# Performance work log

Measured on AMD Instinct MI355X. Metric: run time of the kernel, lower is better.

The kernel has to match this reference:

```python
import jax, jax.numpy as jnp
import numpy as np

N = 100000      # entity nodes
E = 1000000     # edges per relation
D_IN = 256
HID = 128
EPS = 1e-16     # PyG softmax denominator eps
NEG_SLOPE = 0.2 # GATConv default leaky_relu slope


def _gat_conv(x, ei, Ws, Wd, a_s, a_d, b):
    """Single-head GATConv (heads=1, concat=False) with self-loops."""
    n = x.shape[0]
    loop = jnp.arange(n, dtype=ei.dtype)
    src = jnp.concatenate([ei[0], loop])  # [E+N]
    dst = jnp.concatenate([ei[1], loop])
    h_src = x @ Ws                         # [N, HID]
    h_dst = x @ Wd                         # [N, HID]
    a_src = h_src @ a_s                    # [N]
    a_dst = h_dst @ a_d                    # [N]
    e = jax.nn.leaky_relu(a_src[src] + a_dst[dst], NEG_SLOPE)  # [E+N]
    # numerically-stable softmax over incoming edges of each dst node
    m = jax.ops.segment_max(e, dst, num_segments=n)
    ex = jnp.exp(e - m[dst])
    denom = jax.ops.segment_sum(ex, dst, num_segments=n)
    alpha = ex / (denom[dst] + EPS)        # [E+N]
    out = jax.ops.segment_sum(alpha[:, None] * h_src[src], dst, num_segments=n)
    return out + b


def setup_inputs() -> dict:
    key = jax.random.key(0)
    ks = jax.random.split(key, 9)
    s_in = 1.0 / np.sqrt(D_IN)
    s_h = 1.0 / np.sqrt(HID)
    return {
        "x": jax.random.normal(ks[0], (N, D_IN), dtype=jnp.float32),
        "edge_index_r0": jax.random.randint(ks[1], (2, E), 0, N, dtype=jnp.int64)
                         if jax.config.jax_enable_x64 else jax.random.randint(ks[1], (2, E), 0, N).astype(jnp.int32),
        "edge_index_r1": jax.random.randint(ks[2], (2, E), 0, N, dtype=jnp.int64)
                         if jax.config.jax_enable_x64 else jax.random.randint(ks[2], (2, E), 0, N).astype(jnp.int32),
        "W_src": jax.random.normal(ks[3], (2, D_IN, HID), dtype=jnp.float32) * s_in,
        "W_dst": jax.random.normal(ks[4], (2, D_IN, HID), dtype=jnp.float32) * s_in,
        "att_src": jax.random.normal(ks[5], (2, HID), dtype=jnp.float32) * s_h,
        "att_dst": jax.random.normal(ks[6], (2, HID), dtype=jnp.float32) * s_h,
        "bias": jnp.zeros((2, HID), dtype=jnp.float32),
    }


def reference(x, edge_index_r0, edge_index_r1, W_src, W_dst, att_src, att_dst, bias):
    # HeteroConv aggr='sum' over the two entity->entity relations
    out = _gat_conv(x, edge_index_r0, W_src[0], W_dst[0], att_src[0], att_dst[0], bias[0])
    out = out + _gat_conv(x, edge_index_r1, W_src[1], W_dst[1], att_src[1], att_dst[1], bias[1])
    # ELU; dropout p=0.0 is identity
    return jax.nn.elu(out)
```

## Files before the change

### kernel.cpp

```cpp
#include <hip/hip_runtime.h>

typedef __attribute__((ext_vector_type(8))) __bf16 bf16x8;
typedef __attribute__((ext_vector_type(4))) float floatx4;
typedef __attribute__((ext_vector_type(2))) float floatx2;

#define SEG 48

__device__ __forceinline__ float bf2f(unsigned short u) {
    return __uint_as_float(((unsigned)u) << 16);
}
__device__ __forceinline__ unsigned short f2bf(float f) {
    unsigned u = __float_as_uint(f);
    unsigned r = u + 0x7FFFu + ((u >> 16) & 1u);
    return (unsigned short)(r >> 16);
}

__device__ __forceinline__ void canon8(const void* src, unsigned short* dst,
                                       long long idx, int f) {
    if (f) {
        *(uint4*)&dst[idx] = *(const uint4*)((const unsigned short*)src + idx);
    } else {
        const float* sf = (const float*)src;
        unsigned short v[8];
        for (int j = 0; j < 8; ++j) v[j] = f2bf(sf[idx + j]);
        *(uint4*)&dst[idx] = *(const uint4*)v;
    }
}

__global__ __launch_bounds__(256) void detect2_k(
    const unsigned short* __restrict__ xs,
    const void* __restrict__ Ws, const void* __restrict__ Wd,
    const void* __restrict__ as, const void* __restrict__ ad,
    const void* __restrict__ b,
    int* __restrict__ flag, float* __restrict__ vecs,
    unsigned short* __restrict__ bsb) {
    __shared__ int sred[256];
    __shared__ int sflag;
    int tid = threadIdx.x;
    int cnt = 0;
    for (int j = 0; j < 16; ++j) {
        unsigned short u = xs[(tid * 16 + j) * 2];
        int e = (u >> 7) & 0xFF;
        cnt += (e >= 96 && e <= 159) ? 1 : 0;
    }
    sred[tid] = cnt;
    __syncthreads();
    for (int s = 128; s > 0; s >>= 1) {
        if (tid < s) sred[tid] += sred[tid + s];
        __syncthreads();
    }
    if (tid == 0) { sflag = (sred[0] > 2048) ? 1 : 0; *flag = sflag; }
    __syncthreads();
    int f = sflag;
    int k = tid;
    for (int r = 0; r < 2; ++r) {
        float s = 0.f, t = 0.f;
        if (f) {
            const unsigned short* wsrow = (const unsigned short*)Ws + (size_t)r * 32768 + (size_t)k * 128;
            const unsigned short* wdrow = (const unsigned short*)Wd + (size_t)r * 32768 + (size_t)k * 128;
            const unsigned short* asr = (const unsigned short*)as + r * 128;
            const unsigned short* adr = (const unsigned short*)ad + r * 128;
            for (int h = 0; h < 128; ++h) {
                s += bf2f(wsrow[h]) * bf2f(asr[h]);
                t += bf2f(wdrow[h]) * bf2f(adr[h]);
            }
        } else {
            const float* wsrow = (const float*)Ws + (size_t)r * 32768 + (size_t)k * 128;
            const float* wdrow = (const float*)Wd + (size_t)r * 32768 + (size_t)k * 128;
            const float* asr = (const float*)as + r * 128;
            const float* adr = (const float*)ad + r * 128;
            for (int h = 0; h < 128; ++h) {
                s += wsrow[h] * asr[h];
                t += wdrow[h] * adr[h];
            }
        }
        vecs[(r * 2 + 0) * 256 + k] = s;
        vecs[(r * 2 + 1) * 256 + k] = t;
    }
    if (tid < 32) canon8(b, bsb, (long long)tid * 8, f);
}

__global__ __launch_bounds__(256) void pre_k(
    const void* __restrict__ xraw, unsigned short* __restrict__ xb,
    const float* __restrict__ vecs, float* __restrict__ aout, int n, int canB,
    const void* __restrict__ Ws, unsigned short* __restrict__ Bt,
    const int* __restrict__ flag) {
    __shared__ float sv[1024];
    int b = blockIdx.x, tid = threadIdx.x;
    if (b < canB) {
        for (int j = 0; j < 4; ++j) sv[j * 256 + tid] = vecs[j * 256 + tid];
        __syncthreads();
        int lane = tid & 63, wave = tid >> 6;
        int f = *flag;
        for (int rr = 0; rr < 8; ++rr) {
            int row = b * 32 + wave * 8 + rr;
            if (row >= n) break;
            float xf[4];
            if (f) {
                uint2 u = *(const uint2*)((const unsigned short*)xraw + (size_t)row * 256 + lane * 4);
                xf[0] = bf2f((unsigned short)(u.x & 0xFFFF));
                xf[1] = bf2f((unsigned short)(u.x >> 16));
                xf[2] = bf2f((unsigned short)(u.y & 0xFFFF));
                xf[3] = bf2f((unsigned short)(u.y >> 16));
            } else {
                float4 fv = *(const float4*)((const float*)xraw + (size_t)row * 256 + lane * 4);
                xf[0] = fv.x; xf[1] = fv.y; xf[2] = fv.z; xf[3] = fv.w;
                unsigned short v[4] = {f2bf(fv.x), f2bf(fv.y), f2bf(fv.z), f2bf(fv.w)};
                *(uint2*)&xb[(size_t)row * 256 + lane * 4] = *(const uint2*)v;
            }
            float s[4] = {0.f, 0.f, 0.f, 0.f};
            for (int j = 0; j < 4; ++j)
                for (int q = 0; q < 4; ++q)
                    s[j] += xf[q] * sv[j * 256 + lane * 4 + q];
            for (int j = 0; j < 4; ++j)
                for (int off = 32; off > 0; off >>= 1)
                    s[j] += __shfl_down(s[j], off);
            if (lane == 0)
                for (int j = 0; j < 4; ++j) aout[(size_t)j * n + row] = s[j];
        }
        return;
    }
    b -= canB;
    if (b < 256) {
        int i = b * 256 + tid;
        int f = *flag;
        int r = i >> 15, rem = i & 32767;
        int k = rem >> 7, nn = rem & 127;
        unsigned short w = f ? ((const unsigned short*)Ws)[i]
                             : f2bf(((const float*)Ws)[i]);
        Bt[(size_t)r * 32768 + nn * 256 + k] = w;
    }
}

__device__ __forceinline__ void gload_lds16(const void* g, void* l) {
    __builtin_amdgcn_global_load_lds((const __attribute__((address_space(1))) void*)g,
                                     (__attribute__((address_space(3))) void*)l, 16, 0, 0);
}

__global__ __launch_bounds__(256) void gemm_h(const void* __restrict__ x_raw,
                                              const unsigned short* __restrict__ xb,
                                              const unsigned short* __restrict__ Btg,
                                              unsigned short* __restrict__ hout, int n,
                                              const int* __restrict__ flag) {
    const unsigned short* x = (*flag) ? (const unsigned short*)x_raw : xb;
    const int r = blockIdx.y;
    const unsigned short* bt = Btg + (size_t)r * 32768;
    unsigned short* h = hout + (size_t)r * n * 128;
    const int r0 = blockIdx.x * 128;
    __shared__ __align__(16) unsigned short As[128 * 64];
    __shared__ __align__(16) unsigned short Bs[128 * 64];
    int tid = threadIdx.x;
    int lane = tid & 63, wave = tid >> 6;
    int wm = wave >> 1, wn = wave & 1;

    floatx4 acc[4][4];
    for (int mt = 0; mt < 4; ++mt)
        for (int nt = 0; nt < 4; ++nt)
            acc[mt][nt] = (floatx4){0.f, 0.f, 0.f, 0.f};

    int srow = lane >> 3, q = lane & 7;
    int m16 = lane & 15, qb = lane >> 4;

    for (int k0 = 0; k0 < 256; k0 += 64) {
        for (int i = 0; i < 4; ++i) {
            int L = wave * 4 + i;
            int row = L * 8 + srow;
            int sw = ((q ^ (row & 7)) << 3);
            int grow = min(r0 + row, n - 1);
            gload_lds16(x + (size_t)grow * 256 + k0 + sw, &As[L * 512]);
            gload_lds16(bt + (size_t)row * 256 + k0 + sw, &Bs[L * 512]);
        }
        __syncthreads();
        for (int s = 0; s < 2; ++s) {
            int qr = qb + s * 4;
            bf16x8 af[4], bfv[4];
            for (int mt = 0; mt < 4; ++mt) {
                int row = wm * 64 + mt * 16 + m16;
                af[mt] = *(const bf16x8*)&As[row * 64 + ((qr ^ (row & 7)) << 3)];
            }
            for (int nt = 0; nt < 4; ++nt) {
                int row = wn * 64 + nt * 16 + m16;
                bfv[nt] = *(const bf16x8*)&Bs[row * 64 + ((qr ^ (row & 7)) << 3)];
            }
            for (int mt = 0; mt < 4; ++mt)
                for (int nt = 0; nt < 4; ++nt)
                    acc[mt][nt] = __builtin_amdgcn_mfma_f32_16x16x32_bf16(
                        af[mt], bfv[nt], acc[mt][nt], 0, 0, 0);
        }
        __syncthreads();
    }
    for (int mt = 0; mt < 4; ++mt) {
        int baser = r0 + wm * 64 + mt * 16 + qb * 4;
        for (int nt = 0; nt < 4; ++nt) {
            int c = wn * 64 + nt * 16 + m16;
            for (int i = 0; i < 4; ++i) {
                int gr = baser + i;
                if (gr < n) h[(size_t)gr * 128 + c] = f2bf(acc[mt][nt][i]);
            }
        }
    }
}

__global__ void histfill_k(const int* __restrict__ ei0, const int* __restrict__ ei1,
                           const float* __restrict__ avals, int* __restrict__ cnt,
                           unsigned long long* __restrict__ pair0,
                           unsigned long long* __restrict__ pair1,
                           int E_, int n) {
    int rel = blockIdx.y;
    const int* ei = rel ? ei1 : ei0;
    const float* as_ = avals + (rel ? 2 * (size_t)n : 0);
    const float* ad_ = avals + (rel ? 3 * (size_t)n : (size_t)n);
    unsigned long long* pair = rel ? pair1 : pair0;
    int* c = cnt + (rel ? n : 0);
    int t = blockIdx.x * 256 + threadIdx.x;
    if (t >= E_ + n) return;
    int s, d;
    if (t < E_) { s = ei[t]; d = ei[E_ + t]; } else { s = t - E_; d = s; }
    float e = as_[s] + ad_[d];
    e = e > 0.f ? e : 0.2f * e;
    float w = __expf(e);
    int pos;
    if (t < E_) {
        int rank = atomicAdd(&c[d], 1);
        rank = min(rank, SEG - 2);
        pos = d * SEG + 1 + rank;
    } else {
        pos = d * SEG;
    }
    pair[pos] = ((unsigned long long)__float_as_uint(w) << 32) | (unsigned)s;
}

__device__ __forceinline__ void acc8pk(floatx2* a, float w, const uint4& hv) {
    floatx2 wv = {w, w};
    const unsigned u[4] = {hv.x, hv.y, hv.z, hv.w};
#pragma unroll
    for (int k = 0; k < 4; ++k) {
        floatx2 hf;
        hf.x = __uint_as_float(u[k] << 16);
        hf.y = __uint_as_float(u[k] & 0xFFFF0000u);
        asm("v_pk_fma_f32 %0, %1, %2, %0" : "+v"(a[k]) : "v"(wv), "v"(hf));
    }
}

__global__ __launch_bounds__(256) void agg_k(
    const int* __restrict__ cnt,
    const unsigned long long* __restrict__ pair0,
    const unsigned long long* __restrict__ pair1,
    const char* __restrict__ h0, const char* __restrict__ h1,
    const unsigned short* __restrict__ bias, void* __restrict__ out,
    int n, const int* __restrict__ flag) {
    int wave = threadIdx.x >> 6, lane = threadIdx.x & 63;
    int g = lane >> 4, l = lane & 15;
    unsigned l4 = (unsigned)l << 4;
    int d = blockIdx.x * 4 + wave;
    if (d >= n) return;

    int validA = min(cnt[d] + 1, SEG);
    int validB = min(cnt[n + d] + 1, SEG);
    int nIt = (max(validA, validB) + 7) >> 3;
    int i = d * SEG + g;
    int s0 = g, s1 = g + 4;
    unsigned nm1 = (unsigned)(n - 1);

    float denA = 0.f, denB = 0.f;
    floatx2 aA[4], aB[4];
#pragma unroll
    for (int k = 0; k < 4; ++k) {
        aA[k] = (floatx2){0.f, 0.f};
        aB[k] = (floatx2){0.f, 0.f};
    }

    unsigned long long pA0 = pair0[i];
    unsigned long long pA1 = pair0[i + 4];
    unsigned long long pB0 = pair1[i];
    unsigned long long pB1 = pair1[i + 4];

    for (int it = 0; it < nIt; ++it) {
        unsigned xA0 = min((unsigned)pA0, nm1);
        unsigned xA1 = min((unsigned)pA1, nm1);
        unsigned xB0 = min((unsigned)pB0, nm1);
        unsigned xB1 = min((unsigned)pB1, nm1);
        uint4 hA0 = *(const uint4*)(h0 + ((xA0 << 8) + l4));
        uint4 hA1 = *(const uint4*)(h0 + ((xA1 << 8) + l4));
        uint4 hB0 = *(const uint4*)(h1 + ((xB0 << 8) + l4));
        uint4 hB1 = *(const uint4*)(h1 + ((xB1 << 8) + l4));
        float wA0 = (s0 < validA) ? __uint_as_float((unsigned)(pA0 >> 32)) : 0.f;
        float wA1 = (s1 < validA) ? __uint_as_float((unsigned)(pA1 >> 32)) : 0.f;
        float wB0 = (s0 < validB) ? __uint_as_float((unsigned)(pB0 >> 32)) : 0.f;
        float wB1 = (s1 < validB) ? __uint_as_float((unsigned)(pB1 >> 32)) : 0.f;
        i += 8; s0 += 8; s1 += 8;
        pA0 = pair0[i];
        pA1 = pair0[i + 4];
        pB0 = pair1[i];
        pB1 = pair1[i + 4];
        denA += wA0 + wA1;
        denB += wB0 + wB1;
        acc8pk(aA, wA0, hA0);
        acc8pk(aA, wA1, hA1);
        acc8pk(aB, wB0, hB0);
        acc8pk(aB, wB1, hB1);
    }

    denA += __shfl_xor(denA, 16);
    denA += __shfl_xor(denA, 32);
    denB += __shfl_xor(denB, 16);
    denB += __shfl_xor(denB, 32);
    float invA = __builtin_amdgcn_rcpf(denA + 1e-16f);
    float invB = __builtin_amdgcn_rcpf(denB + 1e-16f);
    floatx2 ivA = {invA, invA}, ivB = {invB, invB};
#pragma unroll
    for (int k = 0; k < 4; ++k) {
        asm("v_pk_mul_f32 %0, %0, %1" : "+v"(aA[k]) : "v"(ivA));
        asm("v_pk_fma_f32 %0, %1, %2, %0" : "+v"(aA[k]) : "v"(aB[k]), "v"(ivB));
    }
    float t8[8] = {aA[0].x, aA[0].y, aA[1].x, aA[1].y,
                   aA[2].x, aA[2].y, aA[3].x, aA[3].y};

    uint4 b0 = *(const uint4*)&bias[l * 8];
    uint4 b1 = *(const uint4*)&bias[128 + l * 8];
    const unsigned* b0u = (const unsigned*)&b0;
    const unsigned* b1u = (const unsigned*)&b1;
    float v[8];
#pragma unroll
    for (int j = 0; j < 8; ++j) {
        float s = t8[j];
        s += __shfl_xor(s, 16);
        s += __shfl_xor(s, 32);
        unsigned w0 = b0u[j >> 1], w1 = b1u[j >> 1];
        float bb = bf2f((unsigned short)((j & 1) ? (w0 >> 16) : (w0 & 0xFFFFu)))
                 + bf2f((unsigned short)((j & 1) ? (w1 >> 16) : (w1 & 0xFFFFu)));
        float t = s + bb;
        v[j] = t > 0.f ? t : (__expf(t) - 1.f);
    }
    if (g == 0) {
        if (*flag) {
            unsigned pk[4];
            for (int j = 0; j < 4; ++j)
                pk[j] = ((unsigned)f2bf(v[2 * j + 1]) << 16) | (unsigned)f2bf(v[2 * j]);
            ((uint4*)out)[(size_t)d * 16 + l] = *(const uint4*)pk;
        } else {
            float4 f0 = make_float4(v[0], v[1], v[2], v[3]);
            float4 f1 = make_float4(v[4], v[5], v[6], v[7]);
            ((float4*)out)[(size_t)d * 32 + l * 2] = f0;
            ((float4*)out)[(size_t)d * 32 + l * 2 + 1] = f1;
        }
    }
}

static inline char* carve(char*& p, size_t bytes) {
    char* r = p;
    p += (bytes + 255) & ~(size_t)255;
    return r;
}

extern "C" void kernel_launch(void* const* d_in, const int* in_sizes, int n_in,
                              void* d_out, int out_size, void* d_ws, size_t ws_size,
                              hipStream_t stream) {
    (void)n_in; (void)out_size; (void)ws_size;
    const void* x_raw  = d_in[0];
    const int*  ei0    = (const int*)d_in[1];
    const int*  ei1    = (const int*)d_in[2];
    const void* Ws_raw = d_in[3];
    const void* Wd_raw = d_in[4];
    const void* as_raw = d_in[5];
    const void* ad_raw = d_in[6];
    const void* b_raw  = d_in[7];

    const int n = in_sizes[0] / 256;
    const int e = in_sizes[1] / 2;
    const int tot = e + n;

    char* p = (char*)d_ws;
    float* avals = (float*)carve(p, (size_t)4 * n * 4);
    int*   cnt   = (int*)carve(p, (size_t)2 * n * 4);
    float* vecs  = (float*)carve(p, 1024 * 4);
    int*   flag  = (int*)carve(p, 256);
    unsigned short* xb = (unsigned short*)carve(p, (size_t)(n + 128) * 256 * 2);
    unsigned long long* pair0 = (unsigned long long*)xb;
    unsigned long long* pair1 = (unsigned long long*)carve(p, ((size_t)n * SEG + 64) * 8);
    unsigned short* h0  = (unsigned short*)carve(p, (size_t)2 * n * 128 * 2);
    unsigned short* h1  = h0 + (size_t)n * 128;
    unsigned short* Bt  = (unsigned short*)carve(p, 65536 * 2);
    unsigned short* bsb = (unsigned short*)carve(p, 256 * 2);

    hipMemsetAsync(cnt, 0, (size_t)2 * n * 4, stream);

    detect2_k<<<1, 256, 0, stream>>>((const unsigned short*)x_raw, Ws_raw, Wd_raw,
                                     as_raw, ad_raw, b_raw, flag, vecs, bsb);

    int canB = (n + 31) / 32;
    pre_k<<<canB + 256, 256, 0, stream>>>(x_raw, xb, vecs, avals, n, canB,
                                          Ws_raw, Bt, flag);

    gemm_h<<<dim3((n + 127) / 128, 2), 256, 0, stream>>>(x_raw, xb, Bt, h0, n, flag);

    int gbT = (tot + 255) / 256;
    histfill_k<<<dim3(gbT, 2), 256, 0, stream>>>(ei0, ei1, avals, cnt,
                                                 pair0, pair1, e, n);

    agg_k<<<(n + 3) / 4, 256, 0, stream>>>(cnt, pair0, pair1,
                                           (const char*)h0, (const char*)h1,
                                           bsb, d_out, n, flag);
}
```

Baseline: 436.0 us.

## Merge GEMM and edge histogram-fill into one interleaved launch

The separate GEMM kernel and histogram/pair-fill kernel become one launch. GEMM blocks are spread at a fixed period among the edge-scatter blocks, so compute-bound MFMA work runs alongside the atomic- and memory-bound scatter. pair0 can no longer alias the xb buffer because both run at once, so it gets its own workspace allocation, which uses more memory. The small weight-attention dot products in the detect kernel also switch to vectorised loads.

```diff
diff --git a/kernel.cpp b/kernel.cpp
--- a/kernel.cpp
+++ b/kernel.cpp
@@ -56,22 +56,35 @@
     for (int r = 0; r < 2; ++r) {
         float s = 0.f, t = 0.f;
         if (f) {
-            const unsigned short* wsrow = (const unsigned short*)Ws + (size_t)r * 32768 + (size_t)k * 128;
-            const unsigned short* wdrow = (const unsigned short*)Wd + (size_t)r * 32768 + (size_t)k * 128;
-            const unsigned short* asr = (const unsigned short*)as + r * 128;
-            const unsigned short* adr = (const unsigned short*)ad + r * 128;
-            for (int h = 0; h < 128; ++h) {
-                s += bf2f(wsrow[h]) * bf2f(asr[h]);
-                t += bf2f(wdrow[h]) * bf2f(adr[h]);
+            const uint4* wsr = (const uint4*)((const unsigned short*)Ws + (size_t)r * 32768 + (size_t)k * 128);
+            const uint4* wdr = (const uint4*)((const unsigned short*)Wd + (size_t)r * 32768 + (size_t)k * 128);
+            const uint4* av  = (const uint4*)((const unsigned short*)as + r * 128);
+            const uint4* dv  = (const uint4*)((const unsigned short*)ad + r * 128);
+#pragma unroll 4
+            for (int i = 0; i < 16; ++i) {
+                uint4 w4 = wsr[i], a4 = av[i], v4 = wdr[i], d4 = dv[i];
+                const unsigned* wu = (const unsigned*)&w4;
+                const unsigned* au = (const unsigned*)&a4;
+                const unsigned* vu = (const unsigned*)&v4;
+                const unsigned* du = (const unsigned*)&d4;
+#pragma unroll
+                for (int j = 0; j < 4; ++j) {
+                    s += bf2f((unsigned short)(wu[j] & 0xFFFFu)) * bf2f((unsigned short)(au[j] & 0xFFFFu));
+                    s += bf2f((unsigned short)(wu[j] >> 16))     * bf2f((unsigned short)(au[j] >> 16));
+                    t += bf2f((unsigned short)(vu[j] & 0xFFFFu)) * bf2f((unsigned short)(du[j] & 0xFFFFu));
+                    t += bf2f((unsigned short)(vu[j] >> 16))     * bf2f((unsigned short)(du[j] >> 16));
+                }
             }
         } else {
-            const float* wsrow = (const float*)Ws + (size_t)r * 32768 + (size_t)k * 128;
-            const float* wdrow = (const float*)Wd + (size_t)r * 32768 + (size_t)k * 128;
-            const float* asr = (const float*)as + r * 128;
-            const float* adr = (const float*)ad + r * 128;
-            for (int h = 0; h < 128; ++h) {
-                s += wsrow[h] * asr[h];
-                t += wdrow[h] * adr[h];
+            const float4* wsr = (const float4*)((const float*)Ws + (size_t)r * 32768 + (size_t)k * 128);
+            const float4* wdr = (const float4*)((const float*)Wd + (size_t)r * 32768 + (size_t)k * 128);
+            const float4* av  = (const float4*)((const float*)as + r * 128);
+            const float4* dv  = (const float4*)((const float*)ad + r * 128);
+#pragma unroll 4
+            for (int i = 0; i < 32; ++i) {
+                float4 w4 = wsr[i], a4 = av[i], v4 = wdr[i], d4 = dv[i];
+                s += w4.x * a4.x + w4.y * a4.y + w4.z * a4.z + w4.w * a4.w;
+                t += v4.x * d4.x + v4.y * d4.y + v4.z * d4.z + v4.w * d4.w;
             }
         }
         vecs[(r * 2 + 0) * 256 + k] = s;
@@ -137,83 +150,83 @@
                                      (__attribute__((address_space(3))) void*)l, 16, 0, 0);
 }
 
-__global__ __launch_bounds__(256) void gemm_h(const void* __restrict__ x_raw,
-                                              const unsigned short* __restrict__ xb,
-                                              const unsigned short* __restrict__ Btg,
-                                              unsigned short* __restrict__ hout, int n,
-                                              const int* __restrict__ flag) {
-    const unsigned short* x = (*flag) ? (const unsigned short*)x_raw : xb;
-    const int r = blockIdx.y;
-    const unsigned short* bt = Btg + (size_t)r * 32768;
-    unsigned short* h = hout + (size_t)r * n * 128;
-    const int r0 = blockIdx.x * 128;
+__global__ __launch_bounds__(256) void histgemm_k(
+    const int* __restrict__ ei0, const int* __restrict__ ei1,
+    const float* __restrict__ avals, int* __restrict__ cnt,
+    unsigned long long* __restrict__ pair0, unsigned long long* __restrict__ pair1,
+    int E_, int n, int histB, int period,
+    const void* __restrict__ x_raw, const unsigned short* __restrict__ xb,
+    const unsigned short* __restrict__ Btg, unsigned short* __restrict__ hout,
+    int gemmB, const int* __restrict__ flag) {
     __shared__ __align__(16) unsigned short As[128 * 64];
     __shared__ __align__(16) unsigned short Bs[128 * 64];
-    int tid = threadIdx.x;
-    int lane = tid & 63, wave = tid >> 6;
-    int wm = wave >> 1, wn = wave & 1;
-
-    floatx4 acc[4][4];
-    for (int mt = 0; mt < 4; ++mt)
-        for (int nt = 0; nt < 4; ++nt)
-            acc[mt][nt] = (floatx4){0.f, 0.f, 0.f, 0.f};
-
-    int srow = lane >> 3, q = lane & 7;
-    int m16 = lane & 15, qb = lane >> 4;
-
-    for (int k0 = 0; k0 < 256; k0 += 64) {
-        for (int i = 0; i < 4; ++i) {
-            int L = wave * 4 + i;
-            int row = L * 8 + srow;
-            int sw = ((q ^ (row & 7)) << 3);
-            int grow = min(r0 + row, n - 1);
-            gload_lds16(x + (size_t)grow * 256 + k0 + sw, &As[L * 512]);
-            gload_lds16(bt + (size_t)row * 256 + k0 + sw, &Bs[L * 512]);
+    int b = blockIdx.x, tid = threadIdx.x;
+    int bq = b / period;
+    if (b - bq * period == 0) {
+        if (bq >= gemmB) return;
+        const unsigned short* x = (*flag) ? (const unsigned short*)x_raw : xb;
+        const int r = bq & 1;
+        const unsigned short* bt = Btg + (size_t)r * 32768;
+        unsigned short* h = hout + (size_t)r * n * 128;
+        const int r0 = (bq >> 1) * 128;
+        int lane = tid & 63, wave = tid >> 6;
+        int wm = wave >> 1, wn = wave & 1;
+        floatx4 acc[4][4];
+        for (int mt = 0; mt < 4; ++mt)
+            for (int nt = 0; nt < 4; ++nt)
+                acc[mt][nt] = (floatx4){0.f, 0.f, 0.f, 0.f};
+        int srow = lane >> 3, q = lane & 7;
+        int m16 = lane & 15, qb = lane >> 4;
+        for (int k0 = 0; k0 < 256; k0 += 64) {
+            for (int i = 0; i < 4; ++i) {
+                int L = wave * 4 + i;
+                int row = L * 8 + srow;
+                int sw = ((q ^ (row & 7)) << 3);
+                int grow = min(r0 + row, n - 1);
+                gload_lds16(x + (size_t)grow * 256 + k0 + sw, &As[L * 512]);
+                gload_lds16(bt + (size_t)row * 256 + k0 + sw, &Bs[L * 512]);
+            }
+            __syncthreads();
+            for (int s = 0; s < 2; ++s) {
+                int qr = qb + s * 4;
+                bf16x8 af[4], bfv[4];
+                for (int mt = 0; mt < 4; ++mt) {
+                    int row = wm * 64 + mt * 16 + m16;
+                    af[mt] = *(const bf16x8*)&As[row * 64 + ((qr ^ (row & 7)) << 3)];
+                }
+                for (int nt = 0; nt < 4; ++nt) {
+                    int row = wn * 64 + nt * 16 + m16;
+                    bfv[nt] = *(const bf16x8*)&Bs[row * 64 + ((qr ^ (row & 7)) << 3)];
+                }
+                for (int mt = 0; mt < 4; ++mt)
+                    for (int nt = 0; nt < 4; ++nt)
+                        acc[mt][nt] = __builtin_amdgcn_mfma_f32_16x16x32_bf16(
+                            af[mt], bfv[nt], acc[mt][nt], 0, 0, 0);
+            }
+            __syncthreads();
         }
-        __syncthreads();
-        for (int s = 0; s < 2; ++s) {
-            int qr = qb + s * 4;
-            bf16x8 af[4], bfv[4];
-            for (int mt = 0; mt < 4; ++mt) {
-                int row = wm * 64 + mt * 16 + m16;
-                af[mt] = *(const bf16x8*)&As[row * 64 + ((qr ^ (row & 7)) << 3)];
-            }
+        for (int mt = 0; mt < 4; ++mt) {
+            int baser = r0 + wm * 64 + mt * 16 + qb * 4;
             for (int nt = 0; nt < 4; ++nt) {
-                int row = wn * 64 + nt * 16 + m16;
-                bfv[nt] = *(const bf16x8*)&Bs[row * 64 + ((qr ^ (row & 7)) << 3)];
-            }
-            for (int mt = 0; mt < 4; ++mt)
-                for (int nt = 0; nt < 4; ++nt)
-                    acc[mt][nt] = __builtin_amdgcn_mfma_f32_16x16x32_bf16(
-                        af[mt], bfv[nt], acc[mt][nt], 0, 0, 0);
+                int c = wn * 64 + nt * 16 + m16;
+                for (int i = 0; i < 4; ++i) {
+                    int gr = baser + i;
+                    if (gr < n) h[(size_t)gr * 128 + c] = f2bf(acc[mt][nt][i]);
+                }
+            }
         }
-        __syncthreads();
-    }
-    for (int mt = 0; mt < 4; ++mt) {
-        int baser = r0 + wm * 64 + mt * 16 + qb * 4;
-        for (int nt = 0; nt < 4; ++nt) {
-            int c = wn * 64 + nt * 16 + m16;
-            for (int i = 0; i < 4; ++i) {
-                int gr = baser + i;
-                if (gr < n) h[(size_t)gr * 128 + c] = f2bf(acc[mt][nt][i]);
-            }
-        }
-    }
-}
-
-__global__ void histfill_k(const int* __restrict__ ei0, const int* __restrict__ ei1,
-                           const float* __restrict__ avals, int* __restrict__ cnt,
-                           unsigned long long* __restrict__ pair0,
-                           unsigned long long* __restrict__ pair1,
-                           int E_, int n) {
-    int rel = blockIdx.y;
+        return;
+    }
+    int oid = b - bq - 1;
+    if (oid >= histB) return;
+    int rel = oid & 1;
+    int t = (oid >> 1) * 256 + tid;
+    if (t >= E_ + n) return;
     const int* ei = rel ? ei1 : ei0;
     const float* as_ = avals + (rel ? 2 * (size_t)n : 0);
     const float* ad_ = avals + (rel ? 3 * (size_t)n : (size_t)n);
     unsigned long long* pair = rel ? pair1 : pair0;
     int* c = cnt + (rel ? n : 0);
-    int t = blockIdx.x * 256 + threadIdx.x;
-    if (t >= E_ + n) return;
     int s, d;
     if (t < E_) { s = ei[t]; d = ei[E_ + t]; } else { s = t - E_; d = s; }
     float e = as_[s] + ad_[d];
@@ -376,7 +389,7 @@
     float* vecs  = (float*)carve(p, 1024 * 4);
     int*   flag  = (int*)carve(p, 256);
     unsigned short* xb = (unsigned short*)carve(p, (size_t)(n + 128) * 256 * 2);
-    unsigned long long* pair0 = (unsigned long long*)xb;
+    unsigned long long* pair0 = (unsigned long long*)carve(p, ((size_t)n * SEG + 64) * 8);
     unsigned long long* pair1 = (unsigned long long*)carve(p, ((size_t)n * SEG + 64) * 8);
     unsigned short* h0  = (unsigned short*)carve(p, (size_t)2 * n * 128 * 2);
     unsigned short* h1  = h0 + (size_t)n * 128;
@@ -392,11 +405,14 @@
     pre_k<<<canB + 256, 256, 0, stream>>>(x_raw, xb, vecs, avals, n, canB,
                                           Ws_raw, Bt, flag);
 
-    gemm_h<<<dim3((n + 127) / 128, 2), 256, 0, stream>>>(x_raw, xb, Bt, h0, n, flag);
-
     int gbT = (tot + 255) / 256;
-    histfill_k<<<dim3(gbT, 2), 256, 0, stream>>>(ei0, ei1, avals, cnt,
-                                                 pair0, pair1, e, n);
+    int histB = gbT * 2;
+    int gemmB = ((n + 127) / 128) * 2;
+    int period = (histB + gemmB - 1) / gemmB + 1;
+    int G = gemmB * period;
+    histgemm_k<<<G, 256, 0, stream>>>(
+        ei0, ei1, avals, cnt, pair0, pair1, e, n, histB, period,
+        x_raw, xb, Bt, h0, gemmB, flag);
 
     agg_k<<<(n + 3) / 4, 256, 0, stream>>>(cnt, pair0, pair1,
                                            (const char*)h0, (const char*)h1,
```

Measured after the change: 447.2 us. +2.6%, slower.
